# Kernel optimization log

Measured on AMD Instinct MI355X. Metric: run time of the kernel, lower is better.

The kernel has to match this reference:

```python
import jax, jax.numpy as jnp
import numpy as np

N, E, IN, OUT, R, B = 20000, 640000, 256, 800, 8, 8


def setup_inputs() -> dict:
    key = jax.random.key(0)
    k0, k1, k2, k3, k4, k5 = jax.random.split(key, 6)
    x = jax.random.normal(k0, (N, IN), dtype=jnp.float32)
    edge_index = jax.random.randint(k1, (2, E), 0, N, dtype=jnp.int32)
    edge_type = jax.random.randint(k2, (E,), 0, R, dtype=jnp.int32)
    # basis-decomposed relation weights: W_r = sum_b att[r,b] * bases[b]
    bases = jax.random.normal(k3, (B, IN, OUT), dtype=jnp.float32) * 0.05
    att = jax.random.normal(k4, (R, B), dtype=jnp.float32) * 0.3
    root = jax.random.normal(k5, (IN, OUT), dtype=jnp.float32) * 0.05
    bias = jnp.zeros((OUT,), dtype=jnp.float32)
    return {"x": x, "edge_index": edge_index, "edge_type": edge_type,
            "bases": bases, "att": att, "root": root, "bias": bias}


def reference(x, edge_index, edge_type, bases, att, root, bias):
    # RGCNConv (basis decomposition, scatter-add aggregation):
    #   out[v] = sum_{(u->v, r) in edges} x[u] @ W_r  +  x[v] @ root  +  bias
    # Efficient form: first segment-sum x[src] per (dst, relation), then one
    # dense contraction with the R relation weights (math-identical for add-aggr).
    n, in_dim = x.shape
    r, b = att.shape
    W = jnp.einsum('rb,bio->rio', att, bases)          # [R, IN, OUT]
    src, dst = edge_index[0], edge_index[1]
    seg = dst.astype(jnp.int32) * r + edge_type.astype(jnp.int32)
    # per-(node, relation) sums of source features: [N*R, IN] -> [N, R, IN]
    s = jax.ops.segment_sum(x[src], seg, num_segments=n * r).reshape(n, r, in_dim)
    out = jnp.einsum('nri,rio->no', s, W) + x @ root + bias
    return out
```

## Files before the change

### kernel.cpp

```cpp
#include <hip/hip_runtime.h>


#define N_NODES 20000
#define N_EDGES 640000
#define IN_DIM  256
#define OUT_DIM 800
#define NREL    8
#define NSEG    160000
#define KS      2048
#define KTOT    2304
#define NPAD    1024
#define NB      625

#define BM 256
#define BN 160
#define BK 64
#define NKT (KTOT / BK)
#define MT  79
#define NT  5
#define NWG (MT * NT)
#define ABYTES 32768
#define LBUF 53248

#define XCAST_B (N_NODES * 64 / 256)
#define WCAT_B  ((KTOT / 8) * 4)
#define INIT_NWG (NB + XCAST_B + WCAT_B)

typedef float f32x4_t __attribute__((ext_vector_type(4)));
typedef short short8_t __attribute__((ext_vector_type(8)));

__device__ __forceinline__ unsigned short f2bf(float f) {
  unsigned u = __float_as_uint(f);
  u += 0x7fffu + ((u >> 16) & 1u);
  return (unsigned short)(u >> 16);
}

__device__ __forceinline__ float bflo(unsigned w) { return __uint_as_float(w << 16); }
__device__ __forceinline__ float bfhi(unsigned w) { return __uint_as_float(w & 0xffff0000u); }

__device__ __forceinline__ void gload16(const void* g, void* l) {
  __builtin_amdgcn_global_load_lds(
      (const __attribute__((address_space(1))) void*)g,
      (__attribute__((address_space(3))) void*)l, 16, 0, 0);
}

__global__ void init_kernel(const float* __restrict__ x,
                            const float* __restrict__ bases,
                            const float* __restrict__ att,
                            const float* __restrict__ root,
                            int* __restrict__ cnt,
                            unsigned short* __restrict__ abf,
                            unsigned short* __restrict__ wcatT,
                            unsigned short* __restrict__ xg,
                            int* __restrict__ gtotal) {
  const int b = blockIdx.x;
  const int t = threadIdx.x;
  if (b < NB) {
    cnt[b * 256 + t] = 0;
    if (b == 0 && t == 0) *gtotal = 0;
  } else if (b < NB + XCAST_B) {
    const int id = (b - NB) * 256 + t;
    const int row = id >> 6, lane = id & 63;
    const float4 v = ((const float4*)x)[(size_t)row * 64 + lane];
    union { unsigned short u[4]; uint2 q; } pk;
    pk.u[0] = f2bf(v.x); pk.u[1] = f2bf(v.y);
    pk.u[2] = f2bf(v.z); pk.u[3] = f2bf(v.w);
    *(uint2*)(abf + (size_t)row * KTOT + KS + lane * 4) = pk.q;
    *(uint2*)(xg + (size_t)row * IN_DIM + lane * 4) = pk.q;
  } else {
    const int rem = b - NB - XCAST_B;
    const int kc = rem >> 2, ng = rem & 3;
    const int k0 = kc * 8;
    const int n  = ng * 256 + t;
    if (n >= OUT_DIM) return;
    union { unsigned short u[8]; uint4 q; } pk;
    if (k0 < KS) {
      const int r = k0 >> 8, i0 = k0 & 255;
      float av[8];
      #pragma unroll
      for (int bb = 0; bb < 8; ++bb) av[bb] = att[r * 8 + bb];
      #pragma unroll
      for (int j = 0; j < 8; ++j) {
        float v = 0.f;
        #pragma unroll
        for (int bb = 0; bb < 8; ++bb)
          v += av[bb] * bases[((size_t)bb * IN_DIM + i0 + j) * OUT_DIM + n];
        pk.u[j] = f2bf(v);
      }
    } else {
      #pragma unroll
      for (int j = 0; j < 8; ++j)
        pk.u[j] = f2bf(root[(size_t)(k0 - KS + j) * OUT_DIM + n]);
    }
    *(uint4*)(wcatT + (size_t)n * KTOT + k0) = pk.q;
  }
}


__global__ void hist_kernel(const int* __restrict__ ei, const int* __restrict__ et,
                            int* __restrict__ cnt) {
  const int e0 = (blockIdx.x * 256 + threadIdx.x) * 4;
  const int4 d = *(const int4*)(ei + N_EDGES + e0);
  const int4 r = *(const int4*)(et + e0);
  atomicAdd(&cnt[d.x * NREL + r.x], 1);
  atomicAdd(&cnt[d.y * NREL + r.y], 1);
  atomicAdd(&cnt[d.z * NREL + r.z], 1);
  atomicAdd(&cnt[d.w * NREL + r.w], 1);
}

__global__ void alloc_kernel(const int* __restrict__ cnt, int* __restrict__ off,
                             int* __restrict__ cur, int* __restrict__ gtotal) {
  __shared__ int sm[256];
  __shared__ int sbase;
  const int t = threadIdx.x;
  const int g = blockIdx.x * 256 + t;
  const int v = cnt[g];
  sm[t] = v;
  __syncthreads();
  for (int s = 1; s < 256; s <<= 1) {
    const int a = (t >= s) ? sm[t - s] : 0;
    __syncthreads();
    sm[t] += a;
    __syncthreads();
  }
  if (t == 255) sbase = atomicAdd(gtotal, sm[255]);
  __syncthreads();
  const int ex = sm[t] - v + sbase;
  off[g] = ex;
  cur[g] = ex;
}

__global__ void reorder_kernel(const int* __restrict__ ei, const int* __restrict__ et,
                               int* __restrict__ cur, int* __restrict__ sorted_src) {
  const int e0 = (blockIdx.x * 256 + threadIdx.x) * 4;
  const int4 s = *(const int4*)(ei + e0);
  const int4 d = *(const int4*)(ei + N_EDGES + e0);
  const int4 r = *(const int4*)(et + e0);
  sorted_src[atomicAdd(&cur[d.x * NREL + r.x], 1)] = s.x;
  sorted_src[atomicAdd(&cur[d.y * NREL + r.y], 1)] = s.y;
  sorted_src[atomicAdd(&cur[d.z * NREL + r.z], 1)] = s.z;
  sorted_src[atomicAdd(&cur[d.w * NREL + r.w], 1)] = s.w;
}

__global__ void aggregate_kernel(const int* __restrict__ cnt, const int* __restrict__ off,
                                 const int* __restrict__ sorted_src,
                                 const unsigned short* __restrict__ xg,
                                 unsigned short* __restrict__ abf) {
  const int dst = __builtin_amdgcn_readfirstlane(blockIdx.x * 4 + (threadIdx.x >> 6));
  const int l = threadIdx.x & 63;
  const int half = l >> 5;
  const int sl = l & 31;
  unsigned short* const orow = abf + (size_t)dst * KTOT + sl * 8;

  #pragma unroll 1
  for (int r = 0; r < 8; ++r) {
    const int ne = cnt[dst * 8 + r];
    const int o  = off[dst * 8 + r];
    float a0 = 0.f, a1 = 0.f, a2 = 0.f, a3 = 0.f;
    float a4 = 0.f, a5 = 0.f, a6 = 0.f, a7 = 0.f;
    int j = 0;
    for (; j + 4 <= ne; j += 4) {
      const int s0 = sorted_src[o + j + half];
      const int s1 = sorted_src[o + j + 2 + half];
      const uint4 u = *(const uint4*)(xg + (size_t)s0 * IN_DIM + sl * 8);
      const uint4 v = *(const uint4*)(xg + (size_t)s1 * IN_DIM + sl * 8);
      a0 += bflo(u.x); a1 += bfhi(u.x); a2 += bflo(u.y); a3 += bfhi(u.y);
      a4 += bflo(u.z); a5 += bfhi(u.z); a6 += bflo(u.w); a7 += bfhi(u.w);
      a0 += bflo(v.x); a1 += bfhi(v.x); a2 += bflo(v.y); a3 += bfhi(v.y);
      a4 += bflo(v.z); a5 += bfhi(v.z); a6 += bflo(v.w); a7 += bfhi(v.w);
    }
    for (; j + 2 <= ne; j += 2) {
      const int s = sorted_src[o + j + half];
      const uint4 u = *(const uint4*)(xg + (size_t)s * IN_DIM + sl * 8);
      a0 += bflo(u.x); a1 += bfhi(u.x); a2 += bflo(u.y); a3 += bfhi(u.y);
      a4 += bflo(u.z); a5 += bfhi(u.z); a6 += bflo(u.w); a7 += bfhi(u.w);
    }
    if (j < ne && half == 0) {
      const int s = sorted_src[o + j];
      const uint4 u = *(const uint4*)(xg + (size_t)s * IN_DIM + sl * 8);
      a0 += bflo(u.x); a1 += bfhi(u.x); a2 += bflo(u.y); a3 += bfhi(u.y);
      a4 += bflo(u.z); a5 += bfhi(u.z); a6 += bflo(u.w); a7 += bfhi(u.w);
    }
    a0 += __shfl_xor(a0, 32); a1 += __shfl_xor(a1, 32);
    a2 += __shfl_xor(a2, 32); a3 += __shfl_xor(a3, 32);
    a4 += __shfl_xor(a4, 32); a5 += __shfl_xor(a5, 32);
    a6 += __shfl_xor(a6, 32); a7 += __shfl_xor(a7, 32);
    if (half == 0) {
      union { unsigned short u[8]; uint4 q; } pk;
      pk.u[0] = f2bf(a0); pk.u[1] = f2bf(a1); pk.u[2] = f2bf(a2); pk.u[3] = f2bf(a3);
      pk.u[4] = f2bf(a4); pk.u[5] = f2bf(a5); pk.u[6] = f2bf(a6); pk.u[7] = f2bf(a7);
      *(uint4*)(orow + r * IN_DIM) = pk.q;
    }
  }
}

__global__ __launch_bounds__(512) void gemm_kernel(
    const unsigned short* __restrict__ abf,
    const unsigned short* __restrict__ wcatT,
    const float* __restrict__ bias, float* __restrict__ out) {
  __shared__ __align__(16) char lds[3 * LBUF];

  const int lin = blockIdx.x;
  const int q8 = NWG >> 3, r8 = NWG & 7;
  const int xcd = lin & 7, idx = lin >> 3;
  const int wg = (xcd < r8 ? xcd * (q8 + 1) : r8 * (q8 + 1) + (xcd - r8) * q8) + idx;
  const int row0 = (wg / NT) * BM;
  const int col0 = (wg % NT) * BN;

  const int tid = threadIdx.x;
  const int w = tid >> 6, l = tid & 63;
  const int wm = w >> 1, wn = w & 1;
  const int la = l & 15, lg = l >> 4;
  const int l3 = l >> 3;
  const int sch = (l & 7) ^ l3;

  const unsigned short* gA[4];
  #pragma unroll
  for (int i = 0; i < 4; ++i) {
    int ga = row0 + i * 64 + w * 8 + l3;
    ga = (ga < N_NODES) ? ga : (N_NODES - 1);
    gA[i] = abf + (size_t)ga * KTOT + sch * 8;
  }
  const int b2row = (w < 4) ? (128 + w * 8 + l3) : ((w - 4) * 8 + l3);
  const unsigned short* gB0 = wcatT + (size_t)(col0 + w * 8 + l3) * KTOT + sch * 8;
  const unsigned short* gB1 = wcatT + (size_t)(col0 + 64 + w * 8 + l3) * KTOT + sch * 8;
  const unsigned short* gB2 = wcatT + (size_t)(col0 + b2row) * KTOT + sch * 8;
  const int dB2 = (w < 4) ? (ABYTES + 16384 + w * 1024) : (ABYTES + (w - 4) * 1024);

  f32x4_t acc[4][5];
  #pragma unroll
  for (int i = 0; i < 4; ++i)
    #pragma unroll
    for (int j = 0; j < 5; ++j)
      acc[i][j] = (f32x4_t)(0.0f);

  auto stage_all = [&](int buf, int kt) {
    char* base = lds + buf * LBUF;
    const int ko = kt * BK;
    gload16(gA[0] + ko, base + w * 1024);
    gload16(gA[1] + ko, base + 8192 + w * 1024);
    gload16(gA[2] + ko, base + 16384 + w * 1024);
    gload16(gA[3] + ko, base + 24576 + w * 1024);
    gload16(gB0 + ko, base + ABYTES + w * 1024);
    gload16(gB1 + ko, base + ABYTES + 8192 + w * 1024);
    gload16(gB2 + ko, base + dB2);
  };

  stage_all(0, 0);
  stage_all(1, 1);

  for (int kt = 0; kt < NKT; ++kt) {
    const int cbuf = kt % 3;
    const int pbuf = (kt + 2) % 3;
    const bool pf = (kt + 2) < NKT;
    const int pko = (kt + 2) * BK;
    const char* Ab = lds + cbuf * LBUF;
    const char* Bb = Ab + ABYTES;
    char* pbase = lds + pbuf * LBUF;

    if (kt + 1 < NKT) { asm volatile("s_waitcnt vmcnt(7)" ::: "memory"); }
    else              { asm volatile("s_waitcnt vmcnt(0)" ::: "memory"); }
    __builtin_amdgcn_sched_barrier(0);
    __builtin_amdgcn_s_barrier();

    short8_t af0, af1, af2, af3, bfv[5];

    {
      const int r0 = wm * 64 + la,      r1 = wm * 64 + 16 + la;
      const int r2 = wm * 64 + 32 + la, r3 = wm * 64 + 48 + la;
      af0 = *(const short8_t*)(Ab + r0 * 128 + ((lg << 4) ^ ((r0 & 7) << 4)));
      af1 = *(const short8_t*)(Ab + r1 * 128 + ((lg << 4) ^ ((r1 & 7) << 4)));
      af2 = *(const short8_t*)(Ab + r2 * 128 + ((lg << 4) ^ ((r2 & 7) << 4)));
      af3 = *(const short8_t*)(Ab + r3 * 128 + ((lg << 4) ^ ((r3 & 7) << 4)));
      #pragma unroll
      for (int nf = 0; nf < 5; ++nf) {
        const int rr = wn * 80 + nf * 16 + la;
        bfv[nf] = *(const short8_t*)(Bb + rr * 128 + ((lg << 4) ^ ((rr & 7) << 4)));
      }
      if (pf) { gload16(gA[0] + pko, pbase + w * 1024);
                gload16(gA[1] + pko, pbase + 8192 + w * 1024);
                gload16(gA[2] + pko, pbase + 16384 + w * 1024);
                gload16(gA[3] + pko, pbase + 24576 + w * 1024); }
      __builtin_amdgcn_s_barrier();
      asm volatile("s_waitcnt lgkmcnt(0)" ::: "memory");
      __builtin_amdgcn_sched_barrier(0);
      __builtin_amdgcn_s_setprio(1);
      #pragma unroll
      for (int nf = 0; nf < 5; ++nf)
        acc[0][nf] = __builtin_amdgcn_mfma_f32_16x16x32_bf16(af0, bfv[nf], acc[0][nf], 0, 0, 0);
      #pragma unroll
      for (int nf = 0; nf < 5; ++nf)
        acc[1][nf] = __builtin_amdgcn_mfma_f32_16x16x32_bf16(af1, bfv[nf], acc[1][nf], 0, 0, 0);
      #pragma unroll
      for (int nf = 0; nf < 5; ++nf)
        acc[2][nf] = __builtin_amdgcn_mfma_f32_16x16x32_bf16(af2, bfv[nf], acc[2][nf], 0, 0, 0);
      #pragma unroll
      for (int nf = 0; nf < 5; ++nf)
        acc[3][nf] = __builtin_amdgcn_mfma_f32_16x16x32_bf16(af3, bfv[nf], acc[3][nf], 0, 0, 0);
      __builtin_amdgcn_s_setprio(0);
      __builtin_amdgcn_s_barrier();
    }
    {
      const int r0 = wm * 64 + la,      r1 = wm * 64 + 16 + la;
      const int r2 = wm * 64 + 32 + la, r3 = wm * 64 + 48 + la;
      af0 = *(const short8_t*)(Ab + r0 * 128 + (((4 + lg) << 4) ^ ((r0 & 7) << 4)));
      af1 = *(const short8_t*)(Ab + r1 * 128 + (((4 + lg) << 4) ^ ((r1 & 7) << 4)));
      af2 = *(const short8_t*)(Ab + r2 * 128 + (((4 + lg) << 4) ^ ((r2 & 7) << 4)));
      af3 = *(const short8_t*)(Ab + r3 * 128 + (((4 + lg) << 4) ^ ((r3 & 7) << 4)));
      #pragma unroll
      for (int nf = 0; nf < 5; ++nf) {
        const int rr = wn * 80 + nf * 16 + la;
        bfv[nf] = *(const short8_t*)(Bb + rr * 128 + (((4 + lg) << 4) ^ ((rr & 7) << 4)));
      }
      if (pf) { gload16(gB0 + pko, pbase + ABYTES + w * 1024);
                gload16(gB1 + pko, pbase + ABYTES + 8192 + w * 1024);
                gload16(gB2 + pko, pbase + dB2); }
      __builtin_amdgcn_s_barrier();
      asm volatile("s_waitcnt lgkmcnt(0)" ::: "memory");
      __builtin_amdgcn_sched_barrier(0);
      __builtin_amdgcn_s_setprio(1);
      #pragma unroll
      for (int nf = 0; nf < 5; ++nf)
        acc[0][nf] = __builtin_amdgcn_mfma_f32_16x16x32_bf16(af0, bfv[nf], acc[0][nf], 0, 0, 0);
      #pragma unroll
      for (int nf = 0; nf < 5; ++nf)
        acc[1][nf] = __builtin_amdgcn_mfma_f32_16x16x32_bf16(af1, bfv[nf], acc[1][nf], 0, 0, 0);
      #pragma unroll
      for (int nf = 0; nf < 5; ++nf)
        acc[2][nf] = __builtin_amdgcn_mfma_f32_16x16x32_bf16(af2, bfv[nf], acc[2][nf], 0, 0, 0);
      #pragma unroll
      for (int nf = 0; nf < 5; ++nf)
        acc[3][nf] = __builtin_amdgcn_mfma_f32_16x16x32_bf16(af3, bfv[nf], acc[3][nf], 0, 0, 0);
      __builtin_amdgcn_s_setprio(0);
      __builtin_amdgcn_s_barrier();
    }
  }

  #pragma unroll
  for (int nf = 0; nf < 5; ++nf) {
    const int gcol = col0 + wn * 80 + nf * 16 + la;
    const float bv = bias[gcol];
    #pragma unroll
    for (int f = 0; f < 4; ++f) {
      const int gr0 = row0 + wm * 64 + f * 16 + lg * 4;
      #pragma unroll
      for (int j = 0; j < 4; ++j) {
        const int gr = gr0 + j;
        if (gr < N_NODES)
          out[(size_t)gr * OUT_DIM + gcol] = acc[f][nf][j] + bv;
      }
    }
  }
}

extern "C" void kernel_launch(void* const* d_in, const int* in_sizes, int n_in,
                              void* d_out, int out_size, void* d_ws, size_t ws_size,
                              hipStream_t stream) {
  const float* x     = (const float*)d_in[0];
  const int*   ei    = (const int*)d_in[1];
  const int*   et    = (const int*)d_in[2];
  const float* bases = (const float*)d_in[3];
  const float* att   = (const float*)d_in[4];
  const float* root  = (const float*)d_in[5];
  const float* bias  = (const float*)d_in[6];
  float* out = (float*)d_out;

  char* p = (char*)d_ws;
  unsigned short* abf   = (unsigned short*)p;  p += (size_t)N_NODES * KTOT * 2;
  unsigned short* wcatT = (unsigned short*)p;  p += (size_t)NPAD * KTOT * 2;
  unsigned short* xg    = (unsigned short*)p;  p += (size_t)N_NODES * IN_DIM * 2;
  int* cnt        = (int*)p;                   p += (size_t)NSEG * 4;
  int* off        = (int*)p;                   p += (size_t)NSEG * 4;
  int* cur        = (int*)p;                   p += (size_t)NSEG * 4;
  int* sorted_src = (int*)p;                   p += (size_t)N_EDGES * 4;
  int* gtotal     = (int*)p;                   p += 4096;

  init_kernel<<<INIT_NWG, 256, 0, stream>>>(x, bases, att, root, cnt, abf, wcatT, xg, gtotal);
  hist_kernel<<<N_EDGES / 1024, 256, 0, stream>>>(ei, et, cnt);
  alloc_kernel<<<NB, 256, 0, stream>>>(cnt, off, cur, gtotal);
  reorder_kernel<<<N_EDGES / 1024, 256, 0, stream>>>(ei, et, cur, sorted_src);
  aggregate_kernel<<<N_NODES / 4, 256, 0, stream>>>(cnt, off, sorted_src, xg, abf);
  gemm_kernel<<<NWG, 512, 0, stream>>>(abf, wcatT, bias, out);
}
```

Baseline: 237.2 us.

## Enlarge GEMM M-tile to 448 rows with double-buffered LDS pipeline

```diff
diff --git a/kernel.cpp b/kernel.cpp
--- a/kernel.cpp
+++ b/kernel.cpp
@@ -12,15 +12,15 @@
 #define NPAD    1024
 #define NB      625
 
-#define BM 256
+#define BM 448
 #define BN 160
 #define BK 64
 #define NKT (KTOT / BK)
-#define MT  79
+#define MT  45
 #define NT  5
 #define NWG (MT * NT)
-#define ABYTES 32768
-#define LBUF 53248
+#define ABYTES 57344
+#define LBUF 77824
 
 #define XCAST_B (N_NODES * 64 / 256)
 #define WCAT_B  ((KTOT / 8) * 4)
@@ -198,7 +198,7 @@
     const unsigned short* __restrict__ abf,
     const unsigned short* __restrict__ wcatT,
     const float* __restrict__ bias, float* __restrict__ out) {
-  __shared__ __align__(16) char lds[3 * LBUF];
+  __shared__ __align__(16) char lds[2 * LBUF];
 
   const int lin = blockIdx.x;
   const int q8 = NWG >> 3, r8 = NWG & 7;
@@ -214,9 +214,9 @@
   const int l3 = l >> 3;
   const int sch = (l & 7) ^ l3;
 
-  const unsigned short* gA[4];
+  const unsigned short* gA[7];
   #pragma unroll
-  for (int i = 0; i < 4; ++i) {
+  for (int i = 0; i < 7; ++i) {
     int ga = row0 + i * 64 + w * 8 + l3;
     ga = (ga < N_NODES) ? ga : (N_NODES - 1);
     gA[i] = abf + (size_t)ga * KTOT + sch * 8;
@@ -227,60 +227,59 @@
   const unsigned short* gB2 = wcatT + (size_t)(col0 + b2row) * KTOT + sch * 8;
   const int dB2 = (w < 4) ? (ABYTES + 16384 + w * 1024) : (ABYTES + (w - 4) * 1024);
 
-  f32x4_t acc[4][5];
+  f32x4_t acc[7][5];
   #pragma unroll
-  for (int i = 0; i < 4; ++i)
+  for (int i = 0; i < 7; ++i)
     #pragma unroll
     for (int j = 0; j < 5; ++j)
       acc[i][j] = (f32x4_t)(0.0f);
 
-  auto stage_all = [&](int buf, int kt) {
+  auto stageA = [&](int buf, int kt) {
     char* base = lds + buf * LBUF;
     const int ko = kt * BK;
-    gload16(gA[0] + ko, base + w * 1024);
-    gload16(gA[1] + ko, base + 8192 + w * 1024);
-    gload16(gA[2] + ko, base + 16384 + w * 1024);
-    gload16(gA[3] + ko, base + 24576 + w * 1024);
+    #pragma unroll
+    for (int i = 0; i < 7; ++i)
+      gload16(gA[i] + ko, base + i * 8192 + w * 1024);
+  };
+  auto stageB = [&](int buf, int kt) {
+    char* base = lds + buf * LBUF;
+    const int ko = kt * BK;
     gload16(gB0 + ko, base + ABYTES + w * 1024);
     gload16(gB1 + ko, base + ABYTES + 8192 + w * 1024);
     gload16(gB2 + ko, base + dB2);
   };
 
-  stage_all(0, 0);
-  stage_all(1, 1);
+  stageA(0, 0);
+  stageB(0, 0);
 
   for (int kt = 0; kt < NKT; ++kt) {
-    const int cbuf = kt % 3;
-    const int pbuf = (kt + 2) % 3;
-    const bool pf = (kt + 2) < NKT;
-    const int pko = (kt + 2) * BK;
+    const int cbuf = kt & 1;
+    const int pbuf = cbuf ^ 1;
+    const bool pf = (kt + 1) < NKT;
     const char* Ab = lds + cbuf * LBUF;
     const char* Bb = Ab + ABYTES;
-    char* pbase = lds + pbuf * LBUF;
-
-    if (kt + 1 < NKT) { asm volatile("s_waitcnt vmcnt(7)" ::: "memory"); }
-    else              { asm volatile("s_waitcnt vmcnt(0)" ::: "memory"); }
+
+    asm volatile("s_waitcnt vmcnt(0)" ::: "memory");
     __builtin_amdgcn_sched_barrier(0);
     __builtin_amdgcn_s_barrier();
 
-    short8_t af0, af1, af2, af3, bfv[5];
+    short8_t af0, af1, af2, af3, af4, af5, af6, bfv[5];
 
     {
-      const int r0 = wm * 64 + la,      r1 = wm * 64 + 16 + la;
-      const int r2 = wm * 64 + 32 + la, r3 = wm * 64 + 48 + la;
-      af0 = *(const short8_t*)(Ab + r0 * 128 + ((lg << 4) ^ ((r0 & 7) << 4)));
-      af1 = *(const short8_t*)(Ab + r1 * 128 + ((lg << 4) ^ ((r1 & 7) << 4)));
-      af2 = *(const short8_t*)(Ab + r2 * 128 + ((lg << 4) ^ ((r2 & 7) << 4)));
-      af3 = *(const short8_t*)(Ab + r3 * 128 + ((lg << 4) ^ ((r3 & 7) << 4)));
+      const int rb = wm * 112 + la;
+      af0 = *(const short8_t*)(Ab + (rb      ) * 128 + ((lg << 4) ^ (((rb      ) & 7) << 4)));
+      af1 = *(const short8_t*)(Ab + (rb +  16) * 128 + ((lg << 4) ^ (((rb +  16) & 7) << 4)));
+      af2 = *(const short8_t*)(Ab + (rb +  32) * 128 + ((lg << 4) ^ (((rb +  32) & 7) << 4)));
+      af3 = *(const short8_t*)(Ab + (rb +  48) * 128 + ((lg << 4) ^ (((rb +  48) & 7) << 4)));
+      af4 = *(const short8_t*)(Ab + (rb +  64) * 128 + ((lg << 4) ^ (((rb +  64) & 7) << 4)));
+      af5 = *(const short8_t*)(Ab + (rb +  80) * 128 + ((lg << 4) ^ (((rb +  80) & 7) << 4)));
+      af6 = *(const short8_t*)(Ab + (rb +  96) * 128 + ((lg << 4) ^ (((rb +  96) & 7) << 4)));
       #pragma unroll
       for (int nf = 0; nf < 5; ++nf) {
         const int rr = wn * 80 + nf * 16 + la;
         bfv[nf] = *(const short8_t*)(Bb + rr * 128 + ((lg << 4) ^ ((rr & 7) << 4)));
       }
-      if (pf) { gload16(gA[0] + pko, pbase + w * 1024);
-                gload16(gA[1] + pko, pbase + 8192 + w * 1024);
-                gload16(gA[2] + pko, pbase + 16384 + w * 1024);
-                gload16(gA[3] + pko, pbase + 24576 + w * 1024); }
+      if (pf) stageA(pbuf, kt + 1);
       __builtin_amdgcn_s_barrier();
       asm volatile("s_waitcnt lgkmcnt(0)" ::: "memory");
       __builtin_amdgcn_sched_barrier(0);
@@ -297,24 +296,33 @@
       #pragma unroll
       for (int nf = 0; nf < 5; ++nf)
         acc[3][nf] = __builtin_amdgcn_mfma_f32_16x16x32_bf16(af3, bfv[nf], acc[3][nf], 0, 0, 0);
+      #pragma unroll
+      for (int nf = 0; nf < 5; ++nf)
+        acc[4][nf] = __builtin_amdgcn_mfma_f32_16x16x32_bf16(af4, bfv[nf], acc[4][nf], 0, 0, 0);
+      #pragma unroll
+      for (int nf = 0; nf < 5; ++nf)
+        acc[5][nf] = __builtin_amdgcn_mfma_f32_16x16x32_bf16(af5, bfv[nf], acc[5][nf], 0, 0, 0);
+      #pragma unroll
+      for (int nf = 0; nf < 5; ++nf)
+        acc[6][nf] = __builtin_amdgcn_mfma_f32_16x16x32_bf16(af6, bfv[nf], acc[6][nf], 0, 0, 0);
       __builtin_amdgcn_s_setprio(0);
       __builtin_amdgcn_s_barrier();
     }
     {
-      const int r0 = wm * 64 + la,      r1 = wm * 64 + 16 + la;
-      const int r2 = wm * 64 + 32 + la, r3 = wm * 64 + 48 + la;
-      af0 = *(const short8_t*)(Ab + r0 * 128 + (((4 + lg) << 4) ^ ((r0 & 7) << 4)));
-      af1 = *(const short8_t*)(Ab + r1 * 128 + (((4 + lg) << 4) ^ ((r1 & 7) << 4)));
-      af2 = *(const short8_t*)(Ab + r2 * 128 + (((4 + lg) << 4) ^ ((r2 & 7) << 4)));
-      af3 = *(const short8_t*)(Ab + r3 * 128 + (((4 + lg) << 4) ^ ((r3 & 7) << 4)));
+      const int rb = wm * 112 + la;
+      af0 = *(const short8_t*)(Ab + (rb      ) * 128 + (((4 + lg) << 4) ^ (((rb      ) & 7) << 4)));
+      af1 = *(const short8_t*)(Ab + (rb +  16) * 128 + (((4 + lg) << 4) ^ (((rb +  16) & 7) << 4)));
+      af2 = *(const short8_t*)(Ab + (rb +  32) * 128 + (((4 + lg) << 4) ^ (((rb +  32) & 7) << 4)));
+      af3 = *(const short8_t*)(Ab + (rb +  48) * 128 + (((4 + lg) << 4) ^ (((rb +  48) & 7) << 4)));
+      af4 = *(const short8_t*)(Ab + (rb +  64) * 128 + (((4 + lg) << 4) ^ (((rb +  64) & 7) << 4)));
+      af5 = *(const short8_t*)(Ab + (rb +  80) * 128 + (((4 + lg) << 4) ^ (((rb +  80) & 7) << 4)));
+      af6 = *(const short8_t*)(Ab + (rb +  96) * 128 + (((4 + lg) << 4) ^ (((rb +  96) & 7) << 4)));
       #pragma unroll
       for (int nf = 0; nf < 5; ++nf) {
         const int rr = wn * 80 + nf * 16 + la;
         bfv[nf] = *(const short8_t*)(Bb + rr * 128 + (((4 + lg) << 4) ^ ((rr & 7) << 4)));
       }
-      if (pf) { gload16(gB0 + pko, pbase + ABYTES + w * 1024);
-                gload16(gB1 + pko, pbase + ABYTES + 8192 + w * 1024);
-                gload16(gB2 + pko, pbase + dB2); }
+      if (pf) stageB(pbuf, kt + 1);
       __builtin_amdgcn_s_barrier();
       asm volatile("s_waitcnt lgkmcnt(0)" ::: "memory");
       __builtin_amdgcn_sched_barrier(0);
@@ -331,6 +339,15 @@
       #pragma unroll
       for (int nf = 0; nf < 5; ++nf)
         acc[3][nf] = __builtin_amdgcn_mfma_f32_16x16x32_bf16(af3, bfv[nf], acc[3][nf], 0, 0, 0);
+      #pragma unroll
+      for (int nf = 0; nf < 5; ++nf)
+        acc[4][nf] = __builtin_amdgcn_mfma_f32_16x16x32_bf16(af4, bfv[nf], acc[4][nf], 0, 0, 0);
+      #pragma unroll
+      for (int nf = 0; nf < 5; ++nf)
+        acc[5][nf] = __builtin_amdgcn_mfma_f32_16x16x32_bf16(af5, bfv[nf], acc[5][nf], 0, 0, 0);
+      #pragma unroll
+      for (int nf = 0; nf < 5; ++nf)
+        acc[6][nf] = __builtin_amdgcn_mfma_f32_16x16x32_bf16(af6, bfv[nf], acc[6][nf], 0, 0, 0);
       __builtin_amdgcn_s_setprio(0);
       __builtin_amdgcn_s_barrier();
     }
@@ -341,8 +358,8 @@
     const int gcol = col0 + wn * 80 + nf * 16 + la;
     const float bv = bias[gcol];
     #pragma unroll
-    for (int f = 0; f < 4; ++f) {
-      const int gr0 = row0 + wm * 64 + f * 16 + lg * 4;
+    for (int f = 0; f < 7; ++f) {
+      const int gr0 = row0 + wm * 112 + f * 16 + lg * 4;
       #pragma unroll
       for (int j = 0; j < 4; ++j) {
         const int gr = gr0 + j;
```

Measured after the change: 221.8 us (median of 3 runs). 1.07x faster.
